# Kernel tuning notes

Measured on AMD Instinct MI355X. Metric: run time of the kernel, lower is better.

## Reference

```python
import jax, jax.numpy as jnp
import numpy as np
from math import sqrt

T, B, V = 32, 16, 30000
D, DQKV = 300, 150
K, G = 10, 32            # top-K globals, grapharea_size neighbours each
S = 25000                # last_idx_senses (= SC rows)
EPS = 1e-8


def setup_inputs() -> dict:
    key = jax.random.key(0)
    ks = jax.random.split(key, 6)
    return {
        "predictions_globals": jax.random.normal(ks[0], (T, B, V), jnp.float32),
        "location_context": jax.random.normal(ks[1], (T, B, D), jnp.float32),
        "SC": jax.random.normal(ks[2], (S, D), jnp.float32),
        "Wq": jax.random.normal(ks[3], (D, DQKV), jnp.float32) / sqrt(D),
        "Wk": jax.random.normal(ks[4], (D, DQKV), jnp.float32) / sqrt(D),
        "neighbours_table": jax.random.randint(ks[5], (V, G), 0, S, jnp.int64),
    }


def reference(predictions_globals, location_context, SC, Wq, Wk, neighbours_table):
    # 1) per-sample top-K global selection (sort descending, take K indices)
    _, topk_idx = jax.lax.top_k(predictions_globals, K)          # [T,B,K]
    # 2) sense-neighbour lookup: K globals x G neighbours -> N = K*G senses
    neigh = neighbours_table[topk_idx].reshape(T, B, K * G)      # [T,B,N] int
    # 3) gather precomputed sense contexts
    senses_context = SC[neigh]                                   # [T,B,N,D]
    # 4) ComputeLogits: QK attention logits
    q = location_context @ Wq                                    # [T,B,dqkv]
    k = senses_context @ Wk                                      # [T,B,N,dqkv]
    logits = jnp.einsum("tbd,tbnd->tbn", q, k) / sqrt(DQKV)      # [T,B,N]
    # 5) softmax over neighbours, scatter into full sense distribution
    p = jax.nn.softmax(logits, axis=-1)                          # [T,B,N]
    base = jnp.full((T * B, S), EPS, dtype=p.dtype)
    rows = jnp.arange(T * B)[:, None]                            # [TB,1]
    senses_softmax = base.at[rows, neigh.reshape(T * B, -1)].set(p.reshape(T * B, -1))
    # 6) log-probabilities over all senses
    return jnp.log(senses_softmax)                               # [T*B, S]
```

## Files before the change

### kernel.cpp

```cpp
#include <hip/hip_runtime.h>
#include <math.h>

#define T_ 32
#define B_ 16
#define V_ 30000
#define V4 7500
#define D_ 300
#define DQKV_ 150
#define K_ 10
#define G_ 32
#define N_ 320
#define S_ 25000
#define S4 6250
#define SLICE 3125
#define QKP 304
#define NTS 1024
#define NTG 256
#define NTF 1024
#define LCAP 4096
#define UTH 0xC0000000u

__device__ __forceinline__ unsigned umap(float f) {
    unsigned b = __float_as_uint(f);
    unsigned mask = (unsigned)(((int)b) >> 31);
    return b ^ (mask | 0x80000000u);
}
__device__ __forceinline__ bool better_u(unsigned au, int ai, unsigned bu, int bi) {
    return (au > bu) || (au == bu && ai < bi);
}

__global__ __launch_bounds__(NTS, 2) void stage1_kernel(
    const float* __restrict__ pred, const float* __restrict__ lc,
    const float* __restrict__ Wq, const float* __restrict__ Wk,
    int* __restrict__ wstop, float* __restrict__ qkws)
{
    const int b = blockIdx.x, tid = threadIdx.x;
    const int lane = tid & 63, wave = tid >> 6;
    __shared__ unsigned lu[LCAP];
    __shared__ int      li[LCAP];
    __shared__ int      cnt;
    __shared__ unsigned wcv[16 * K_];
    __shared__ int      wci[16 * K_];
    __shared__ __align__(16) float lcs[D_];
    __shared__ float    qpart[2][DQKV_];

    if (b >= T_ * B_) {
        const int row = b - T_ * B_;
        if (tid < D_ / 4)
            ((float4*)lcs)[tid] = ((const float4*)(lc + (size_t)row * D_))[tid];
        __syncthreads();

        if (tid < 2 * DQKV_) {
            int h = tid / DQKV_;
            int j = tid - h * DQKV_;
            int d0 = h * 150;
            const float* wp = Wq + (size_t)d0 * DQKV_ + j;
            float a0 = 0.f, a1 = 0.f;
            #pragma unroll 5
            for (int dd = 0; dd < 150; dd += 2) {
                a0 += lcs[d0 + dd]     * wp[(size_t)dd * DQKV_];
                a1 += lcs[d0 + dd + 1] * wp[(size_t)(dd + 1) * DQKV_];
            }
            qpart[h][j] = a0 + a1;
        }
        __syncthreads();

        float qv0 = qpart[0][lane] + qpart[1][lane];
        float qv1 = qpart[0][64 + lane] + qpart[1][64 + lane];
        float qv2 = (lane < 22) ? (qpart[0][128 + lane] + qpart[1][128 + lane]) : 0.f;
        for (int d = wave; d < D_; d += 16) {
            const float* wr = Wk + (size_t)d * DQKV_;
            float w0 = wr[lane];
            float w1 = wr[64 + lane];
            float w2 = (lane < 22) ? wr[128 + lane] : 0.f;
            float p = w0 * qv0 + w1 * qv1 + w2 * qv2;
            #pragma unroll
            for (int off = 32; off; off >>= 1) p += __shfl_xor(p, off, 64);
            if (lane == 0) qkws[(size_t)row * QKP + d] = p;
        }
        return;
    }

    const int row = b;
    if (tid == 0) cnt = 0;
    __syncthreads();

    {
        const float4* p4 = (const float4*)(pred + (size_t)row * V_);
        const float4 NEG = make_float4(-INFINITY, -INFINITY, -INFINITY, -INFINITY);
        float4 a[8]; int ib[8]; bool okf[8];
        #pragma unroll
        for (int u = 0; u < 8; ++u) {
            int i = tid + u * NTS;
            okf[u] = i < V4;
            a[u]  = okf[u] ? p4[i] : NEG;
            ib[u] = i * 4;
        }
        const unsigned long long lmask = (lane == 63) ? 0x7fffffffffffffffull
                                                      : ((1ull << lane) - 1ull);
        #pragma unroll
        for (int u = 0; u < 8; ++u) {
            float vals[4] = {a[u].x, a[u].y, a[u].z, a[u].w};
            #pragma unroll
            for (int c = 0; c < 4; ++c) {
                unsigned uu = umap(vals[c]);
                bool has = okf[u] && (uu >= UTH);
                unsigned long long mask = __ballot(has);
                if (mask) {
                    int bs = 0;
                    if (lane == 0) bs = atomicAdd(&cnt, (int)__popcll(mask));
                    bs = __shfl(bs, 0, 64);
                    if (has) {
                        int p = bs + (int)__popcll(mask & lmask);
                        if (p < LCAP) { lu[p] = uu; li[p] = ib[u] + c; }
                    }
                }
            }
        }
    }
    __syncthreads();
    const int c = cnt;
    const bool mainpath = (c >= K_ && c <= LCAP);

    if (mainpath) {
        unsigned cu[4]; int cix[4];
        #pragma unroll
        for (int k = 0; k < 4; ++k) {
            int s = wave * 64 + lane + k * NTS;
            bool ok = s < c;
            cu[k]  = ok ? lu[s] : 0u;
            cix[k] = ok ? li[s] : 0x7fffffff;
        }
        for (int p = 0; p < K_; ++p) {
            unsigned bu = cu[0]; int bi = cix[0];
            #pragma unroll
            for (int k = 1; k < 4; ++k)
                if (better_u(cu[k], cix[k], bu, bi)) { bu = cu[k]; bi = cix[k]; }
            #pragma unroll
            for (int off = 32; off; off >>= 1) {
                unsigned ou = __shfl_xor(bu, off, 64);
                int      oi = __shfl_xor(bi, off, 64);
                if (better_u(ou, oi, bu, bi)) { bu = ou; bi = oi; }
            }
            if (lane == 0) { wcv[wave * K_ + p] = bu; wci[wave * K_ + p] = bi; }
            #pragma unroll
            for (int k = 0; k < 4; ++k)
                if (cix[k] == bi) cu[k] = 0u;
        }
        __syncthreads();

        if (wave == 0) {
            unsigned c0u = wcv[lane],      c1u = wcv[64 + lane];
            int      c0i = wci[lane],      c1i = wci[64 + lane];
            unsigned c2u = (lane < 32) ? wcv[128 + lane] : 0u;
            int      c2i = (lane < 32) ? wci[128 + lane] : 0x7fffffff;
            for (int p = 0; p < K_; ++p) {
                unsigned bu = c0u; int bi = c0i;
                if (better_u(c1u, c1i, bu, bi)) { bu = c1u; bi = c1i; }
                if (better_u(c2u, c2i, bu, bi)) { bu = c2u; bi = c2i; }
                #pragma unroll
                for (int off = 32; off; off >>= 1) {
                    unsigned ou = __shfl_xor(bu, off, 64);
                    int      oi = __shfl_xor(bi, off, 64);
                    if (better_u(ou, oi, bu, bi)) { bu = ou; bi = oi; }
                }
                if (lane == 0) wstop[row * K_ + p] = bi;
                if (c0i == bi) c0u = 0u;
                if (c1i == bi) c1u = 0u;
                if (c2i == bi) c2u = 0u;
            }
        }
    } else {
        if (wave == 0) {
            unsigned tu[K_]; int tix[K_];
            #pragma unroll
            for (int s = 0; s < K_; ++s) { tu[s] = 0; tix[s] = 0x7fffffff; }
            const float* prow = pred + (size_t)row * V_;
            for (int i = lane; i < V_; i += 64) {
                unsigned u = umap(prow[i]);
                if (better_u(u, i, tu[K_-1], tix[K_-1])) {
                    tu[K_-1] = u; tix[K_-1] = i;
                    #pragma unroll
                    for (int s = K_-1; s > 0; --s)
                        if (better_u(tu[s], tix[s], tu[s-1], tix[s-1])) {
                            unsigned a = tu[s]; tu[s] = tu[s-1]; tu[s-1] = a;
                            int b2 = tix[s]; tix[s] = tix[s-1]; tix[s-1] = b2;
                        }
                }
            }
            for (int p = 0; p < K_; ++p) {
                unsigned bu = tu[0]; int bi = tix[0];
                #pragma unroll
                for (int s = 1; s < K_; ++s)
                    if (better_u(tu[s], tix[s], bu, bi)) { bu = tu[s]; bi = tix[s]; }
                #pragma unroll
                for (int off = 32; off; off >>= 1) {
                    unsigned ou = __shfl_xor(bu, off, 64);
                    int      oi = __shfl_xor(bi, off, 64);
                    if (better_u(ou, oi, bu, bi)) { bu = ou; bi = oi; }
                }
                if (lane == 0) wstop[row * K_ + p] = bi;
                #pragma unroll
                for (int s = 0; s < K_; ++s)
                    if (tix[s] == bi) tu[s] = 0;
            }
        }
    }
}

__global__ __launch_bounds__(NTG) void gather_kernel(
    const float* __restrict__ SC, const float* __restrict__ qkws,
    const int* __restrict__ nbt, const int* __restrict__ wstop,
    float* __restrict__ logws)
{
    const int r = blockIdx.x >> 3;
    const int ch = blockIdx.x & 7;
    const int lo = ch * SLICE, hi = lo + SLICE;
    const int tid = threadIdx.x;
    __shared__ int   topg[K_];
    __shared__ int   nid[N_];
    __shared__ __align__(16) float qk[D_];
    __shared__ int   list[N_];
    __shared__ int   lcnt;

    if (tid == 0) lcnt = 0;
    if (tid < K_) topg[tid] = wstop[r * K_ + tid];
    if (tid >= 64 && tid < 64 + D_ / 4)
        ((float4*)qk)[tid - 64] = ((const float4*)(qkws + (size_t)r * QKP))[tid - 64];
    __syncthreads();

    for (int i = tid; i < N_; i += NTG)
        nid[i] = nbt[topg[i >> 5] * G_ + (i & 31)];
    __syncthreads();

    for (int i = tid; i < N_; i += NTG) {
        int sv = nid[i];
        if (sv >= lo && sv < hi) { int p = atomicAdd(&lcnt, 1); list[p] = i; }
    }
    __syncthreads();
    const int c2 = lcnt;

    const float ISC = 0.08164965809277260327f;
    const float4* q4 = (const float4*)qk;
    for (int s = tid; s < 8 * c2; s += NTG) {
        int g = s >> 3, h = s & 7;
        int n = list[g];
        const float4* sc4 = (const float4*)(SC + (size_t)nid[n] * D_);
        int c0 = h * 9;
        float acc = 0.f;
        #pragma unroll
        for (int cc = 0; cc < 9; ++cc) {
            float4 a = sc4[c0 + cc];
            float4 bq = q4[c0 + cc];
            acc += a.x * bq.x + a.y * bq.y + a.z * bq.z + a.w * bq.w;
        }
        if (h < 3) {
            float4 a = sc4[72 + h];
            float4 bq = q4[72 + h];
            acc += a.x * bq.x + a.y * bq.y + a.z * bq.z + a.w * bq.w;
        }
        acc += __shfl_xor(acc, 1, 64);
        acc += __shfl_xor(acc, 2, 64);
        acc += __shfl_xor(acc, 4, 64);
        if (h == 0) logws[(size_t)r * N_ + n] = acc * ISC;
    }
}

__global__ __launch_bounds__(NTF) void finalize_kernel(
    const float* __restrict__ logws, const int* __restrict__ nbt,
    const int* __restrict__ wstop, float* __restrict__ out)
{
    const int row = blockIdx.x, tid = threadIdx.x;
    const int lane = tid & 63, wave = tid >> 6;
    __shared__ int   topg[K_];
    __shared__ float lg[N_];
    __shared__ int   nid[N_];
    __shared__ int   kills[N_];
    __shared__ float redA[16], redB[16];
    float* outrow = out + (size_t)row * S_;

    const float FILL = -18.420680743952367f;
    {
        float4 f4 = make_float4(FILL, FILL, FILL, FILL);
        float4* o4 = (float4*)outrow;
        #pragma unroll
        for (int k = 0; k < 7; ++k) { int i = tid + k * NTF; if (i < S4) o4[i] = f4; }
    }

    if (tid < K_) topg[tid] = wstop[row * K_ + tid];
    __syncthreads();
    if (tid < N_) {
        nid[tid] = nbt[topg[tid >> 5] * G_ + (tid & 31)];
        lg[tid]  = logws[(size_t)row * N_ + tid];
        kills[tid] = 0;
    }
    __syncthreads();

    float v = (tid < N_) ? lg[tid] : -INFINITY;
    float m = v;
    #pragma unroll
    for (int off = 32; off; off >>= 1) m = fmaxf(m, __shfl_xor(m, off, 64));
    if (lane == 0) redA[wave] = m;
    __syncthreads();
    m = redA[0];
    #pragma unroll
    for (int w = 1; w < 16; ++w) m = fmaxf(m, redA[w]);

    float ss = (tid < N_) ? expf(v - m) : 0.f;
    #pragma unroll
    for (int off = 32; off; off >>= 1) ss += __shfl_xor(ss, off, 64);
    if (lane == 0) redB[wave] = ss;
    __syncthreads();
    float tot = redB[0];
    #pragma unroll
    for (int w = 1; w < 16; ++w) tot += redB[w];
    float lsum = logf(tot);

    for (int s = tid; s < 4 * N_; s += NTF) {
        int n = s >> 2, cix = s & 3;
        int sidx = nid[n];
        int clo = cix * 80;
        int lo2 = (n + 1 > clo) ? n + 1 : clo;
        int hi2 = clo + 80;
        bool mt = false;
        #pragma unroll 4
        for (int n2 = lo2; n2 < hi2; ++n2) mt |= (nid[n2] == sidx);
        if (mt) kills[n] = 1;
    }
    __syncthreads();

    if (tid < N_ && !kills[tid]) outrow[nid[tid]] = (v - m) - lsum;
}

#define NWS 16
__device__ __forceinline__ bool better(float av, int ai, float bv, int bi) {
    return (av > bv) || (av == bv && ai < bi);
}
__global__ __launch_bounds__(NTS, 4) void selfatt_fused(
    const float* __restrict__ pred, const float* __restrict__ lc,
    const float* __restrict__ SC, const float* __restrict__ Wq,
    const float* __restrict__ Wk, const int* __restrict__ nbt,
    float* __restrict__ out)
{
    const int row = blockIdx.x, tid = threadIdx.x;
    const int lane = tid & 63, wave = tid >> 6;
    __shared__ float wcv[NWS * K_];
    __shared__ int   wci[NWS * K_];
    __shared__ int   topg[K_];
    __shared__ float lcs[D_];
    __shared__ float qs[DQKV_];
    __shared__ __align__(16) float qks[D_];
    __shared__ int   nidx[N_];
    __shared__ float lg[N_];
    __shared__ int   kills[N_];
    __shared__ float redA[NWS], redB[NWS];
    float* outrow = out + (size_t)row * S_;
    const float FILL = -18.420680743952367f;
    {
        float4 f4 = make_float4(FILL, FILL, FILL, FILL);
        float4* o4 = (float4*)outrow;
        #pragma unroll
        for (int k = 0; k < 7; ++k) { int i = tid + k * NTS; if (i < S4) o4[i] = f4; }
    }
    float tv[K_]; int ti[K_];
    #pragma unroll
    for (int s = 0; s < K_; ++s) { tv[s] = -INFINITY; ti[s] = 0x7fffffff; }
    {
        const float4* p4 = (const float4*)(pred + (size_t)row * V_);
        const float4 NEG = make_float4(-INFINITY, -INFINITY, -INFINITY, -INFINITY);
        float4 a[8]; int ib[8];
        #pragma unroll
        for (int u = 0; u < 8; ++u) {
            int i = tid + u * NTS;
            a[u]  = (i < V4) ? p4[i] : NEG;
            ib[u] = (i < V4) ? i * 4 : 0x7ffffff0;
        }
        #pragma unroll
        for (int u = 0; u < 8; ++u) {
            float x = a[u].x, y = a[u].y, z = a[u].z, w = a[u].w;
            float m4 = fmaxf(fmaxf(x, y), fmaxf(z, w));
            if (!(m4 < tv[K_-1])) {
                float vals[4] = {x, y, z, w};
                #pragma unroll
                for (int cc = 0; cc < 4; ++cc) {
                    float val = vals[cc];
                    int   idx = ib[u] + cc;
                    if (better(val, idx, tv[K_-1], ti[K_-1])) {
                        tv[K_-1] = val; ti[K_-1] = idx;
                        #pragma unroll
                        for (int s = K_-1; s > 0; --s) {
                            if (better(tv[s], ti[s], tv[s-1], ti[s-1])) {
                                float fx = tv[s]; tv[s] = tv[s-1]; tv[s-1] = fx;
                                int   iy = ti[s]; ti[s] = ti[s-1]; ti[s-1] = iy;
                            }
                        }
                    }
                }
            }
        }
    }
    for (int p = 0; p < K_; ++p) {
        float bv = tv[0]; int bi = ti[0];
        #pragma unroll
        for (int s = 1; s < K_; ++s)
            if (better(tv[s], ti[s], bv, bi)) { bv = tv[s]; bi = ti[s]; }
        #pragma unroll
        for (int off = 32; off; off >>= 1) {
            float ov = __shfl_xor(bv, off, 64);
            int   oi = __shfl_xor(bi, off, 64);
            if (better(ov, oi, bv, bi)) { bv = ov; bi = oi; }
        }
        if (lane == 0) { wcv[wave * K_ + p] = bv; wci[wave * K_ + p] = bi; }
        #pragma unroll
        for (int s = 0; s < K_; ++s)
            if (ti[s] == bi) tv[s] = -INFINITY;
    }
    __syncthreads();
    if (wave == 0) {
        float c0v = wcv[lane],      c1v = wcv[64 + lane];
        int   c0i = wci[lane],      c1i = wci[64 + lane];
        float c2v = (lane < 32) ? wcv[128 + lane] : -INFINITY;
        int   c2i = (lane < 32) ? wci[128 + lane] : 0x7fffffff;
        for (int p = 0; p < K_; ++p) {
            float bv = c0v; int bi = c0i;
            if (better(c1v, c1i, bv, bi)) { bv = c1v; bi = c1i; }
            if (better(c2v, c2i, bv, bi)) { bv = c2v; bi = c2i; }
            #pragma unroll
            for (int off = 32; off; off >>= 1) {
                float ov = __shfl_xor(bv, off, 64);
                int   oi = __shfl_xor(bi, off, 64);
                if (better(ov, oi, bv, bi)) { bv = ov; bi = oi; }
            }
            if (lane == 0) topg[p] = bi;
            if (c0i == bi) c0v = -INFINITY;
            if (c1i == bi) c1v = -INFINITY;
            if (c2i == bi) c2v = -INFINITY;
        }
    }
    __syncthreads();
    if (tid < N_) { int g = topg[tid >> 5]; nidx[tid] = nbt[g * G_ + (tid & 31)]; }
    else if (tid < 2 * N_) kills[tid - N_] = 0;
    else if (tid >= 640 && tid < 640 + D_) lcs[tid - 640] = lc[(size_t)row * D_ + (tid - 640)];
    __syncthreads();
    if (tid < 600) {
        int j = tid >> 2, h = tid & 3;
        int d0 = h * 75;
        const float* wp = Wq + (size_t)d0 * DQKV_ + j;
        float acc = 0.f;
        #pragma unroll 5
        for (int dd = 0; dd < 75; ++dd) acc += lcs[d0 + dd] * wp[(size_t)dd * DQKV_];
        acc += __shfl_xor(acc, 1, 64);
        acc += __shfl_xor(acc, 2, 64);
        if (h == 0) qs[j] = acc;
    } else {
        int t0 = tid - 600;
        for (int s = t0; s < 4 * N_; s += 424) {
            int n = s >> 2, cc = s & 3;
            int sidx = nidx[n];
            int clo = cc * 80;
            int lo = (n + 1 > clo) ? n + 1 : clo;
            int hi = clo + 80;
            bool mt = false;
            #pragma unroll 4
            for (int n2 = lo; n2 < hi; ++n2) mt |= (nidx[n2] == sidx);
            if (mt) kills[n] = 1;
        }
    }
    __syncthreads();
    if (tid < 600) {
        int d = tid >> 1, h = tid & 1;
        int j0 = h * 75;
        const float* wrow = Wk + (size_t)d * DQKV_ + j0;
        float acc = 0.f;
        #pragma unroll 5
        for (int jj = 0; jj < 75; ++jj) acc += wrow[jj] * qs[j0 + jj];
        acc += __shfl_xor(acc, 1, 64);
        if (h == 0) qks[d] = acc;
    }
    __syncthreads();
    const float ISC = 0.08164965809277260327f;
    const float4* q4 = (const float4*)qks;
    for (int s = tid; s < 8 * N_; s += NTS) {
        int n = s >> 3, h = s & 7;
        const float4* sc4 = (const float4*)(SC + (size_t)nidx[n] * D_);
        int c0 = h * 9;
        float acc = 0.f;
        #pragma unroll
        for (int cc = 0; cc < 9; ++cc) {
            float4 a = sc4[c0 + cc];
            float4 b = q4[c0 + cc];
            acc += a.x * b.x + a.y * b.y + a.z * b.z + a.w * b.w;
        }
        if (h < 3) {
            float4 a = sc4[72 + h];
            float4 b = q4[72 + h];
            acc += a.x * b.x + a.y * b.y + a.z * b.z + a.w * b.w;
        }
        acc += __shfl_xor(acc, 1, 64);
        acc += __shfl_xor(acc, 2, 64);
        acc += __shfl_xor(acc, 4, 64);
        if (h == 0) lg[n] = acc * ISC;
    }
    __syncthreads();
    float v = (tid < N_) ? lg[tid] : -INFINITY;
    float m = v;
    #pragma unroll
    for (int off = 32; off; off >>= 1) m = fmaxf(m, __shfl_xor(m, off, 64));
    if (lane == 0) redA[wave] = m;
    __syncthreads();
    m = redA[0];
    #pragma unroll
    for (int w = 1; w < NWS; ++w) m = fmaxf(m, redA[w]);
    float e = (tid < N_) ? expf(v - m) : 0.f;
    float ss = e;
    #pragma unroll
    for (int off = 32; off; off >>= 1) ss += __shfl_xor(ss, off, 64);
    if (lane == 0) redB[wave] = ss;
    __syncthreads();
    float tot = redB[0];
    #pragma unroll
    for (int w = 1; w < NWS; ++w) tot += redB[w];
    float lsum = logf(tot);
    if (tid < N_ && !kills[tid]) outrow[nidx[tid]] = (v - m) - lsum;
}

extern "C" void kernel_launch(void* const* d_in, const int* in_sizes, int n_in,
                              void* d_out, int out_size, void* d_ws, size_t ws_size,
                              hipStream_t stream) {
    const float* pred = (const float*)d_in[0];
    const float* lc   = (const float*)d_in[1];
    const float* SC   = (const float*)d_in[2];
    const float* Wq   = (const float*)d_in[3];
    const float* Wk   = (const float*)d_in[4];
    const int*   nbt  = (const int*)d_in[5];
    float* out = (float*)d_out;

    const int nrows = T_ * B_;
    const size_t nQK = (size_t)nrows * QKP;
    const size_t nLG = (size_t)nrows * N_;
    const size_t nTP = (size_t)nrows * K_;
    const size_t need = (nQK + nLG) * sizeof(float) + nTP * sizeof(int);

    if (ws_size >= need) {
        float* qkws  = (float*)d_ws;
        float* logws = qkws + nQK;
        int*   wstop = (int*)(logws + nLG);
        stage1_kernel<<<dim3(nrows * 2), dim3(NTS), 0, stream>>>(
            pred, lc, Wq, Wk, wstop, qkws);
        gather_kernel<<<dim3(nrows * 8), dim3(NTG), 0, stream>>>(
            SC, qkws, nbt, wstop, logws);
        finalize_kernel<<<dim3(nrows), dim3(NTF), 0, stream>>>(
            logws, nbt, wstop, out);
    } else {
        selfatt_fused<<<dim3(nrows), dim3(NTS), 0, stream>>>(
            pred, lc, SC, Wq, Wk, nbt, out);
    }
}
```

Measured before the change: 105.0 us.

## Move output fill into gather kernel and replace atomic compaction with prefix scan

The EPS fill of the 25000-wide output rows now runs inside the gather kernel, split across its 8 chunk blocks per row, so the finalize kernel only scatters and can use 384 threads. The top-K candidate compaction in stage1 replaces per-ballot LDS atomics with per-thread counts, a wave prefix scan and a cross-wave sum. The fill is meant to overlap with the gather's SC loads, and the scan removes atomic contention. The finalize kernel's scatter still depends on stream ordering after gather, and candidate order in the list changes, which is harmless because ties break on index.

Measured after the change: 104.5 us. No clear change (-0.5%).

```diff
diff --git a/kernel.cpp b/kernel.cpp
--- a/kernel.cpp
+++ b/kernel.cpp
@@ -16,7 +16,7 @@
 #define QKP 304
 #define NTS 1024
 #define NTG 256
-#define NTF 1024
+#define NTF 384
 #define LCAP 4096
 #define UTH 0xC0000000u
 
@@ -38,7 +38,7 @@
     const int lane = tid & 63, wave = tid >> 6;
     __shared__ unsigned lu[LCAP];
     __shared__ int      li[LCAP];
-    __shared__ int      cnt;
+    __shared__ int      wtot[16];
     __shared__ unsigned wcv[16 * K_];
     __shared__ int      wci[16 * K_];
     __shared__ __align__(16) float lcs[D_];
@@ -82,44 +82,57 @@
     }
 
     const int row = b;
-    if (tid == 0) cnt = 0;
-    __syncthreads();
-
-    {
-        const float4* p4 = (const float4*)(pred + (size_t)row * V_);
-        const float4 NEG = make_float4(-INFINITY, -INFINITY, -INFINITY, -INFINITY);
-        float4 a[8]; int ib[8]; bool okf[8];
-        #pragma unroll
-        for (int u = 0; u < 8; ++u) {
-            int i = tid + u * NTS;
-            okf[u] = i < V4;
-            a[u]  = okf[u] ? p4[i] : NEG;
-            ib[u] = i * 4;
-        }
-        const unsigned long long lmask = (lane == 63) ? 0x7fffffffffffffffull
-                                                      : ((1ull << lane) - 1ull);
-        #pragma unroll
-        for (int u = 0; u < 8; ++u) {
-            float vals[4] = {a[u].x, a[u].y, a[u].z, a[u].w};
-            #pragma unroll
-            for (int c = 0; c < 4; ++c) {
-                unsigned uu = umap(vals[c]);
-                bool has = okf[u] && (uu >= UTH);
-                unsigned long long mask = __ballot(has);
-                if (mask) {
-                    int bs = 0;
-                    if (lane == 0) bs = atomicAdd(&cnt, (int)__popcll(mask));
-                    bs = __shfl(bs, 0, 64);
-                    if (has) {
-                        int p = bs + (int)__popcll(mask & lmask);
-                        if (p < LCAP) { lu[p] = uu; li[p] = ib[u] + c; }
-                    }
-                }
-            }
-        }
-    }
-    __syncthreads();
-    const int c = cnt;
+
+    const float4* p4 = (const float4*)(pred + (size_t)row * V_);
+    const float4 NEG = make_float4(-INFINITY, -INFINITY, -INFINITY, -INFINITY);
+    float4 a[8]; int ib[8]; bool okf[8];
+    #pragma unroll
+    for (int u = 0; u < 8; ++u) {
+        int i = tid + u * NTS;
+        okf[u] = i < V4;
+        a[u]  = okf[u] ? p4[i] : NEG;
+        ib[u] = i * 4;
+    }
+
+    int nc = 0;
+    #pragma unroll
+    for (int u = 0; u < 8; ++u) {
+        nc += (okf[u] && umap(a[u].x) >= UTH);
+        nc += (okf[u] && umap(a[u].y) >= UTH);
+        nc += (okf[u] && umap(a[u].z) >= UTH);
+        nc += (okf[u] && umap(a[u].w) >= UTH);
+    }
+
+    int incl = nc;
+    #pragma unroll
+    for (int d = 1; d < 64; d <<= 1) {
+        int t = __shfl_up(incl, d, 64);
+        if (lane >= d) incl += t;
+    }
+    if (lane == 63) wtot[wave] = incl;
+    __syncthreads();
+
+    int wbase = 0, c = 0;
+    #pragma unroll
+    for (int w = 0; w < 16; ++w) {
+        int t = wtot[w];
+        if (w < wave) wbase += t;
+        c += t;
+    }
+    int pos = wbase + (incl - nc);
+
+    #pragma unroll
+    for (int u = 0; u < 8; ++u) {
+        float vals[4] = {a[u].x, a[u].y, a[u].z, a[u].w};
+        #pragma unroll
+        for (int cc = 0; cc < 4; ++cc) {
+            unsigned uu = umap(vals[cc]);
+            if (okf[u] && uu >= UTH && pos < LCAP) {
+                lu[pos] = uu; li[pos] = ib[u] + cc; ++pos;
+            }
+        }
+    }
+    __syncthreads();
     const bool mainpath = (c >= K_ && c <= LCAP);
 
     if (mainpath) {
@@ -183,7 +196,7 @@
                     #pragma unroll
                     for (int s = K_-1; s > 0; --s)
                         if (better_u(tu[s], tix[s], tu[s-1], tix[s-1])) {
-                            unsigned a = tu[s]; tu[s] = tu[s-1]; tu[s-1] = a;
+                            unsigned aa = tu[s]; tu[s] = tu[s-1]; tu[s-1] = aa;
                             int b2 = tix[s]; tix[s] = tix[s-1]; tix[s-1] = b2;
                         }
                 }
@@ -211,7 +224,7 @@
 __global__ __launch_bounds__(NTG) void gather_kernel(
     const float* __restrict__ SC, const float* __restrict__ qkws,
     const int* __restrict__ nbt, const int* __restrict__ wstop,
-    float* __restrict__ logws)
+    float* __restrict__ out, float* __restrict__ logws)
 {
     const int r = blockIdx.x >> 3;
     const int ch = blockIdx.x & 7;
@@ -223,6 +236,14 @@
     __shared__ int   list[N_];
     __shared__ int   lcnt;
 
+    const float FILL = -18.420680743952367f;
+    {
+        int f4lo = (ch * S4) >> 3, f4hi = ((ch + 1) * S4) >> 3;
+        float4 f4 = make_float4(FILL, FILL, FILL, FILL);
+        float4* o4 = (float4*)(out + (size_t)r * S_);
+        for (int i = f4lo + tid; i < f4hi; i += NTG) o4[i] = f4;
+    }
+
     if (tid == 0) lcnt = 0;
     if (tid < K_) topg[tid] = wstop[r * K_ + tid];
     if (tid >= 64 && tid < 64 + D_ / 4)
@@ -250,14 +271,14 @@
         float acc = 0.f;
         #pragma unroll
         for (int cc = 0; cc < 9; ++cc) {
-            float4 a = sc4[c0 + cc];
+            float4 av = sc4[c0 + cc];
             float4 bq = q4[c0 + cc];
-            acc += a.x * bq.x + a.y * bq.y + a.z * bq.z + a.w * bq.w;
+            acc += av.x * bq.x + av.y * bq.y + av.z * bq.z + av.w * bq.w;
         }
         if (h < 3) {
-            float4 a = sc4[72 + h];
+            float4 av = sc4[72 + h];
             float4 bq = q4[72 + h];
-            acc += a.x * bq.x + a.y * bq.y + a.z * bq.z + a.w * bq.w;
+            acc += av.x * bq.x + av.y * bq.y + av.z * bq.z + av.w * bq.w;
         }
         acc += __shfl_xor(acc, 1, 64);
         acc += __shfl_xor(acc, 2, 64);
@@ -276,16 +297,8 @@
     __shared__ float lg[N_];
     __shared__ int   nid[N_];
     __shared__ int   kills[N_];
-    __shared__ float redA[16], redB[16];
+    __shared__ float redA[6], redB[6];
     float* outrow = out + (size_t)row * S_;
-
-    const float FILL = -18.420680743952367f;
-    {
-        float4 f4 = make_float4(FILL, FILL, FILL, FILL);
-        float4* o4 = (float4*)outrow;
-        #pragma unroll
-        for (int k = 0; k < 7; ++k) { int i = tid + k * NTF; if (i < S4) o4[i] = f4; }
-    }
 
     if (tid < K_) topg[tid] = wstop[row * K_ + tid];
     __syncthreads();
@@ -304,7 +317,7 @@
     __syncthreads();
     m = redA[0];
     #pragma unroll
-    for (int w = 1; w < 16; ++w) m = fmaxf(m, redA[w]);
+    for (int w = 1; w < 6; ++w) m = fmaxf(m, redA[w]);
 
     float ss = (tid < N_) ? expf(v - m) : 0.f;
     #pragma unroll
@@ -313,7 +326,7 @@
     __syncthreads();
     float tot = redB[0];
     #pragma unroll
-    for (int w = 1; w < 16; ++w) tot += redB[w];
+    for (int w = 1; w < 6; ++w) tot += redB[w];
     float lsum = logf(tot);
 
     for (int s = tid; s < 4 * N_; s += NTF) {
@@ -548,7 +561,7 @@
         stage1_kernel<<<dim3(nrows * 2), dim3(NTS), 0, stream>>>(
             pred, lc, Wq, Wk, wstop, qkws);
         gather_kernel<<<dim3(nrows * 8), dim3(NTG), 0, stream>>>(
-            SC, qkws, nbt, wstop, logws);
+            SC, qkws, nbt, wstop, out, logws);
         finalize_kernel<<<dim3(nrows), dim3(NTF), 0, stream>>>(
             logws, nbt, wstop, out);
     } else {
```
